# Kernel optimization log

Hardware: AMD Instinct MI355X
Metric: run time of the kernel (lower is better)

Reference implementation:

```python
import jax, jax.numpy as jnp
import numpy as np

D_MODEL = 1024
NUM_HEADS = 16
HEAD_DIM = D_MODEL // NUM_HEADS

def _trunc_normal(key, shape, std=0.02, a=-0.04, b=0.04):
    u = jax.random.truncated_normal(key, a / std, b / std, shape, dtype=jnp.float32)
    return u * std

def setup_inputs() -> dict:
    key = jax.random.key(0)
    kx, kq, kk, kv, ko = jax.random.split(key, 5)
    x = jax.random.normal(kx, (4, 2048, D_MODEL), dtype=jnp.float32)
    Wq = _trunc_normal(kq, (D_MODEL, D_MODEL))
    Wk = _trunc_normal(kk, (D_MODEL, D_MODEL))
    Wv = _trunc_normal(kv, (D_MODEL, D_MODEL))
    Wo = _trunc_normal(ko, (D_MODEL, D_MODEL))
    return {"x": x, "Wq": Wq, "Wk": Wk, "Wv": Wv, "Wo": Wo}

def reference(x, Wq, Wk, Wv, Wo):
    B, S, D = x.shape
    H, Dh = NUM_HEADS, HEAD_DIM
    # projections: x @ W.T
    Q = jnp.einsum('bsd,ed->bse', x, Wq).reshape(B, S, H, Dh).transpose(0, 2, 1, 3)
    K = jnp.einsum('bsd,ed->bse', x, Wk).reshape(B, S, H, Dh).transpose(0, 2, 1, 3)
    V = jnp.einsum('bsd,ed->bse', x, Wv).reshape(B, S, H, Dh).transpose(0, 2, 1, 3)
    scale = 1.0 / jnp.sqrt(jnp.asarray(Dh, dtype=x.dtype))
    scores = jnp.einsum('bhqd,bhkd->bhqk', Q, K) * scale  # [B,H,S,S]
    causal = jnp.tril(jnp.ones((S, S), dtype=bool))  # True where attend allowed
    scores = jnp.where(causal, scores, -jnp.inf)
    attn = jax.nn.softmax(scores, axis=-1)
    ctx = jnp.einsum('bhqk,bhkd->bhqd', attn, V)  # [B,H,S,Dh]
    ctx = ctx.transpose(0, 2, 1, 3).reshape(B, S, D)
    out = jnp.einsum('bsd,ed->bse', ctx, Wo)
    return out
```

## Files before the change

kernel.cpp:

```cpp
#include <hip/hip_runtime.h>

#define D_MODEL 1024
#define SEQ 2048
#define BATCH 4
#define HEADS 16
#define HDIM 64

typedef short bf16x8 __attribute__((ext_vector_type(8)));
typedef float f32x4 __attribute__((ext_vector_type(4)));

#define FENCE() asm volatile("" ::: "memory")

__device__ __forceinline__ unsigned short f2bf(float f) {
  union { float f; unsigned int u; } c; c.f = f;
  unsigned int u = c.u;
  unsigned int r = (u + 0x7FFFu + ((u >> 16) & 1u)) >> 16;
  return (unsigned short)r;
}

__device__ __forceinline__ unsigned int cvt_pk_bf16(float a, float b) {
  unsigned int r;
  asm("v_cvt_pk_bf16_f32 %0, %1, %2" : "=v"(r) : "v"(a), "v"(b));
  return r;
}

__device__ __forceinline__ float exp2_hw(float x) {
  float r;
  asm("v_exp_f32 %0, %1" : "=v"(r) : "v"(x));
  return r;
}

__device__ __forceinline__ void async16(const void* g, const void* lds) {
  __builtin_amdgcn_global_load_lds((const __attribute__((address_space(1))) void*)g,
                                   (__attribute__((address_space(3))) void*)lds, 16, 0, 0);
}

__global__ void cvt_all(const float* __restrict__ x,
                        const float* __restrict__ Wq, const float* __restrict__ Wk,
                        const float* __restrict__ Wv, const float* __restrict__ Wo,
                        unsigned short* __restrict__ xb,
                        unsigned short* __restrict__ Wqkv,
                        unsigned short* __restrict__ Wob) {
  int bid = blockIdx.x;
  const float* s;
  unsigned short* d;
  int i;
  if (bid < 8192) {
    s = x; d = xb; i = bid * 256 + threadIdx.x;
  } else {
    int b = (bid - 8192) >> 10;
    i = ((bid - 8192) & 1023) * 256 + threadIdx.x;
    s = (b == 0) ? Wq : (b == 1) ? Wk : (b == 2) ? Wv : Wo;
    d = (b == 3) ? Wob : (Wqkv + b * (D_MODEL * D_MODEL));
  }
  float4 v = ((const float4*)s)[i];
  ushort4 o;
  o.x = f2bf(v.x); o.y = f2bf(v.y); o.z = f2bf(v.z); o.w = f2bf(v.w);
  ((ushort4*)d)[i] = o;
}

__global__ __launch_bounds__(512, 2) void gemm256qk(
    const unsigned short* __restrict__ A, const unsigned short* __restrict__ Bw,
    unsigned short* __restrict__ Qd, unsigned short* __restrict__ Kd) {
  __shared__ unsigned short At[2][256 * 64];
  __shared__ unsigned short Bt[2][256 * 64];
  const int t = threadIdx.x;
  const int lane = t & 63;
  const int wid = t >> 6;
  const int wm = wid >> 2;
  const int wn = wid & 3;

  const int gx = gridDim.x;
  const int nwg = gridDim.x * gridDim.y;
  int flat = blockIdx.y * gx + blockIdx.x;
  flat = (flat & 7) * (nwg >> 3) + (flat >> 3);
  const int m0 = (flat / gx) * 256;
  const int n0 = (flat % gx) * 256;

  const int K = 1024;
  f32x4 acc[8][4] = {};

  const int srow = t >> 3;
  const int scol = ((t & 7) ^ (srow & 7)) << 3;
  const unsigned short* Ags = A + (size_t)(m0 + srow) * K + scol;
  const unsigned short* Bgs = Bw + (size_t)(n0 + srow) * K + scol;

  const int l15 = lane & 15;
  const int lh = lane >> 4;
  const int rsw = (l15 & 7) << 4;
  const int cb0 = (lh * 16) ^ rsw;
  const int cb1 = (64 + lh * 16) ^ rsw;
  const int aBase = (wm * 128 + l15) * 128;
  const int bBase = (wn * 64 + l15) * 128;

#define STG_A(o, c, kn) async16(Ags + (size_t)(c) * 64 * K + (kn), &At[o][(c) * 4096 + t * 8])
#define STG_B(o, c, kn) async16(Bgs + (size_t)(c) * 64 * K + (kn), &Bt[o][(c) * 4096 + t * 8])

  STG_B(0, 0, 0); STG_B(0, 1, 0); STG_B(0, 2, 0); STG_B(0, 3, 0);
  STG_A(0, 0, 0); STG_A(0, 1, 0); STG_A(0, 2, 0); STG_A(0, 3, 0);
  asm volatile("s_waitcnt vmcnt(0)" ::: "memory");
  __builtin_amdgcn_s_barrier();
  FENCE();

  for (int kt = 0; kt < K; kt += 64) {
    const int s = (kt >> 6) & 1;
    const int o = s ^ 1;
    const int kn = kt + 64;
    const bool more = kn < K;
    const char* Ab = (const char*)&At[s][0];
    const char* Bb = (const char*)&Bt[s][0];

    bf16x8 bfr[4][2];
#pragma unroll
    for (int p = 0; p < 4; ++p) {
      bf16x8 af[2][2];
#pragma unroll
      for (int i = 0; i < 2; ++i) {
        af[i][0] = *(const bf16x8*)(Ab + aBase + (2 * p + i) * 2048 + cb0);
        af[i][1] = *(const bf16x8*)(Ab + aBase + (2 * p + i) * 2048 + cb1);
      }
      if (p == 0) {
#pragma unroll
        for (int fn = 0; fn < 4; ++fn) {
          bfr[fn][0] = *(const bf16x8*)(Bb + bBase + fn * 2048 + cb0);
          bfr[fn][1] = *(const bf16x8*)(Bb + bBase + fn * 2048 + cb1);
        }
        if (more) { STG_B(o, 0, kn); STG_B(o, 1, kn); }
      } else if (p == 1) {
        if (more) { STG_B(o, 2, kn); STG_B(o, 3, kn); }
      } else if (p == 2) {
        if (more) { STG_A(o, 0, kn); STG_A(o, 2, kn); }
      } else {
        if (more) { STG_A(o, 1, kn); STG_A(o, 3, kn); }
      }
      __builtin_amdgcn_s_barrier();
      FENCE();
      __builtin_amdgcn_s_setprio(1);
#pragma unroll
      for (int ks = 0; ks < 2; ++ks)
#pragma unroll
        for (int i = 0; i < 2; ++i)
#pragma unroll
          for (int fn = 0; fn < 4; ++fn)
            acc[2 * p + i][fn] = __builtin_amdgcn_mfma_f32_16x16x32_bf16(
                af[i][ks], bfr[fn][ks], acc[2 * p + i][fn], 0, 0, 0);
      __builtin_amdgcn_s_setprio(0);
      FENCE();
      if (p == 1) {
        if (more) asm volatile("s_waitcnt vmcnt(4)" ::: "memory");
        else      asm volatile("s_waitcnt vmcnt(0)" ::: "memory");
      } else if (p == 3) {
        if (more) asm volatile("s_waitcnt vmcnt(2)" ::: "memory");
        else      asm volatile("s_waitcnt vmcnt(0)" ::: "memory");
      }
      __builtin_amdgcn_s_barrier();
      FENCE();
    }
  }
#undef STG_A
#undef STG_B

#pragma unroll
  for (int fm = 0; fm < 8; ++fm) {
#pragma unroll
    for (int fn = 0; fn < 4; ++fn) {
#pragma unroll
      for (int r = 0; r < 4; ++r) {
        float v = acc[fm][fn][r];
        int m = m0 + wm * 128 + fm * 16 + lh * 4 + r;
        int n = n0 + wn * 64 + fn * 16 + l15;
        int p = n >> 10;
        int h = (n >> 6) & 15;
        int dh = n & 63;
        int b = m >> 11;
        int sx = m & 2047;
        unsigned short* dst = (p == 0) ? Qd : Kd;
        if (p == 0) v *= 0.18033688011112042f;
        dst[(((size_t)(b * HEADS + h)) * SEQ + sx) * HDIM + dh] = f2bf(v);
      }
    }
  }
}

template <int MODE>
__global__ __launch_bounds__(512, 1) void gemm128(
    const unsigned short* __restrict__ A, const unsigned short* __restrict__ Bw,
    int nOfs, unsigned short* __restrict__ Vtd, float* __restrict__ Od) {
  __shared__ unsigned short At[2][128 * 64];
  __shared__ unsigned short Bt[2][256 * 64];
  const int t = threadIdx.x;
  const int lane = t & 63;
  const int wid = t >> 6;
  const int wm = wid >> 1;
  const int wn = wid & 1;

  const int gx = gridDim.x;
  const int nwg = gridDim.x * gridDim.y;
  int flat = blockIdx.y * gx + blockIdx.x;
  flat = (flat & 7) * (nwg >> 3) + (flat >> 3);
  const int m0 = (flat / gx) * 128;
  const int n0 = nOfs + (flat % gx) * 256;

  const int K = 1024;
  f32x4 acc[2][8] = {};

  const int srow = t >> 3;
  const int scol = ((t & 7) ^ (srow & 7)) << 3;
  const unsigned short* Ags = A + (size_t)(m0 + srow) * K + scol;
  const unsigned short* Bgs = Bw + (size_t)(n0 + srow) * K + scol;

  const int l15 = lane & 15;
  const int lh = lane >> 4;
  const int rsw = (l15 & 7) << 4;
  const int cb0 = (lh * 16) ^ rsw;
  const int cb1 = (64 + lh * 16) ^ rsw;
  const int aBase = (wm * 32 + l15) * 128;
  const int bBase = (wn * 128 + l15) * 128;

#define STG_A(o, c, kn) async16(Ags + (size_t)(c) * 64 * K + (kn), &At[o][(c) * 4096 + t * 8])
#define STG_B(o, c, kn) async16(Bgs + (size_t)(c) * 64 * K + (kn), &Bt[o][(c) * 4096 + t * 8])

  STG_A(0, 0, 0); STG_A(0, 1, 0); STG_B(0, 0, 0); STG_B(0, 2, 0);
  STG_B(0, 1, 0); STG_B(0, 3, 0);
  asm volatile("s_waitcnt vmcnt(0)" ::: "memory");
  __builtin_amdgcn_s_barrier();
  FENCE();

  for (int kt = 0; kt < K; kt += 64) {
    const int s = (kt >> 6) & 1;
    const int o = s ^ 1;
    const int kn = kt + 64;
    const bool more = kn < K;
    const char* Ab = (const char*)&At[s][0];
    const char* Bb = (const char*)&Bt[s][0];

    bf16x8 af[2][2];
#pragma unroll
    for (int p = 0; p < 4; ++p) {
      if (p == 0) {
#pragma unroll
        for (int i = 0; i < 2; ++i) {
          af[i][0] = *(const bf16x8*)(Ab + aBase + i * 2048 + cb0);
          af[i][1] = *(const bf16x8*)(Ab + aBase + i * 2048 + cb1);
        }
      }
      bf16x8 bfr[2][2];
#pragma unroll
      for (int j = 0; j < 2; ++j) {
        bfr[j][0] = *(const bf16x8*)(Bb + bBase + (2 * p + j) * 2048 + cb0);
        bfr[j][1] = *(const bf16x8*)(Bb + bBase + (2 * p + j) * 2048 + cb1);
      }
      if (p == 0)      { if (more) { STG_A(o, 0, kn); STG_A(o, 1, kn); } }
      else if (p == 1) { if (more) { STG_B(o, 0, kn); STG_B(o, 2, kn); } }
      else if (p == 2) { if (more) { STG_B(o, 1, kn); STG_B(o, 3, kn); } }
      __builtin_amdgcn_s_barrier();
      FENCE();
      __builtin_amdgcn_s_setprio(1);
#pragma unroll
      for (int ks = 0; ks < 2; ++ks)
#pragma unroll
        for (int i = 0; i < 2; ++i)
#pragma unroll
          for (int j = 0; j < 2; ++j) {
            if (MODE == 1)
              acc[i][2 * p + j] = __builtin_amdgcn_mfma_f32_16x16x32_bf16(
                  bfr[j][ks], af[i][ks], acc[i][2 * p + j], 0, 0, 0);
            else
              acc[i][2 * p + j] = __builtin_amdgcn_mfma_f32_16x16x32_bf16(
                  af[i][ks], bfr[j][ks], acc[i][2 * p + j], 0, 0, 0);
          }
      __builtin_amdgcn_s_setprio(0);
      FENCE();
      if (p == 1) {
        if (more) asm volatile("s_waitcnt vmcnt(4)" ::: "memory");
        else      asm volatile("s_waitcnt vmcnt(0)" ::: "memory");
      } else if (p == 3) {
        if (more) asm volatile("s_waitcnt vmcnt(2)" ::: "memory");
        else      asm volatile("s_waitcnt vmcnt(0)" ::: "memory");
      }
      __builtin_amdgcn_s_barrier();
      FENCE();
    }
  }
#undef STG_A
#undef STG_B

#pragma unroll
  for (int fm = 0; fm < 2; ++fm) {
#pragma unroll
    for (int fn = 0; fn < 8; ++fn) {
#pragma unroll
      for (int r = 0; r < 4; ++r) {
        float v = acc[fm][fn][r];
        if (MODE == 1) {
          int n = n0 + wn * 128 + fn * 16 + lh * 4 + r;
          int m = m0 + wm * 32 + fm * 16 + l15;
          int h = (n >> 6) & 15;
          int d = n & 63;
          int b = m >> 11;
          int s = m & 2047;
          Vtd[(((size_t)(b * HEADS + h)) * HDIM + d) * SEQ + s] = f2bf(v);
        } else {
          int m = m0 + wm * 32 + fm * 16 + lh * 4 + r;
          int n = n0 + wn * 128 + fn * 16 + l15;
          Od[(size_t)m * D_MODEL + n] = v;
        }
      }
    }
  }
}

__global__ __launch_bounds__(256, 3) void attn_fwd(
    const unsigned short* __restrict__ Qg, const unsigned short* __restrict__ Kg,
    const unsigned short* __restrict__ Vtg, unsigned short* __restrict__ Cg) {
  __shared__ unsigned short Kl[128 * 64];
  __shared__ unsigned short Vl[64 * 128];
  __shared__ unsigned short Pl[4][32 * 72];
  char* KlB = (char*)Kl;
  char* VlB = (char*)Vl;

  const int t = threadIdx.x;
  const int lane = t & 63;
  const int wq = t >> 6;
  const int bh = blockIdx.x;
  const int q0 = (15 - blockIdx.y) * 128;
  const size_t base = (size_t)bh * SEQ * HDIM;
  const unsigned short* Qb = Qg + base;
  const unsigned short* Kb = Kg + base;
  const unsigned short* Vb = Vtg + base;
  char* PlB = (char*)&Pl[wq][0];

  const int l15 = lane & 15;
  const int lh = lane >> 4;
  const int qrow = q0 + wq * 32;

  bf16x8 qf[2][2];
#pragma unroll
  for (int fm = 0; fm < 2; ++fm)
#pragma unroll
    for (int ks = 0; ks < 2; ++ks)
      qf[fm][ks] = *(const bf16x8*)&Qb[(size_t)(qrow + fm * 16 + l15) * HDIM +
                                       ks * 32 + lh * 8];

  f32x4 acc[2][4] = {};
  float lpart[2] = {0.f, 0.f};

  const int srow = t >> 3;
  const int sc8 = ((t & 7) ^ (srow & 7)) << 3;
  const int srowV = t >> 4;
  const int scV8 = (((t & 15) ^ (srowV & 7)) << 3);

  const int kv_end = q0 + 128;
  for (int kvb = 0; kvb < kv_end; kvb += 128) {
    __syncthreads();
#pragma unroll
    for (int i = 0; i < 4; ++i)
      async16(Kb + (size_t)(kvb + i * 32 + srow) * HDIM + sc8, &Kl[i * 2048 + t * 8]);
#pragma unroll
    for (int i = 0; i < 4; ++i)
      async16(Vb + (size_t)(i * 16 + srowV) * SEQ + kvb + scV8, &Vl[i * 2048 + t * 8]);
    asm volatile("s_waitcnt vmcnt(0)" ::: "memory");
    __syncthreads();

#pragma unroll
    for (int kh = 0; kh < 2; ++kh) {
      const int kv0 = kvb + kh * 64;
      if (kv0 > qrow + 31) continue;

      f32x4 sfr[2][4] = {};
#pragma unroll
      for (int ks = 0; ks < 2; ++ks) {
        bf16x8 kf[4];
#pragma unroll
        for (int fn = 0; fn < 4; ++fn) {
          int row = kh * 64 + fn * 16 + l15;
          kf[fn] = *(const bf16x8*)&KlB[row * 128 +
                                        ((ks * 64 + lh * 16) ^ ((row & 7) << 4))];
        }
#pragma unroll
        for (int fm = 0; fm < 2; ++fm)
#pragma unroll
          for (int fn = 0; fn < 4; ++fn)
            sfr[fm][fn] = __builtin_amdgcn_mfma_f32_16x16x32_bf16(
                kf[fn], qf[fm][ks], sfr[fm][fn], 0, 0, 0);
      }

      const bool need_mask = (kv0 + 63) > qrow;
#pragma unroll
      for (int fm = 0; fm < 2; ++fm) {
        const int q = qrow + fm * 16 + l15;
        float p[4][4];
#pragma unroll
        for (int fn = 0; fn < 4; ++fn)
#pragma unroll
          for (int r = 0; r < 4; ++r) p[fn][r] = sfr[fm][fn][r];
        if (need_mask) {
#pragma unroll
          for (int fn = 0; fn < 4; ++fn)
#pragma unroll
            for (int r = 0; r < 4; ++r) {
              int key = kv0 + fn * 16 + lh * 4 + r;
              if (key > q) p[fn][r] = -1e30f;
            }
        }
        float st = 0.f;
#pragma unroll
        for (int fn = 0; fn < 4; ++fn)
#pragma unroll
          for (int r = 0; r < 4; ++r) {
            p[fn][r] = exp2_hw(p[fn][r]);
            st += p[fn][r];
          }
        lpart[fm] += st;

#pragma unroll
        for (int fn = 0; fn < 4; ++fn) {
#pragma unroll
          for (int w = 0; w < 2; ++w) {
            unsigned int pk = cvt_pk_bf16(p[fn][2 * w], p[fn][2 * w + 1]);
            *(unsigned int*)&PlB[(fm * 16 + l15) * 144 + fn * 32 + lh * 8 + w * 4] = pk;
          }
        }
      }

#pragma unroll
      for (int ks = 0; ks < 2; ++ks) {
        bf16x8 pf[2], vf[4];
#pragma unroll
        for (int fm = 0; fm < 2; ++fm)
          pf[fm] = *(const bf16x8*)&PlB[(fm * 16 + l15) * 144 + ks * 64 + lh * 16];
#pragma unroll
        for (int fn = 0; fn < 4; ++fn) {
          int row = fn * 16 + l15;
          vf[fn] = *(const bf16x8*)&VlB[row * 256 +
                                        ((kh * 128 + ks * 64 + lh * 16) ^ ((row & 7) << 4))];
        }
#pragma unroll
        for (int fm = 0; fm < 2; ++fm)
#pragma unroll
          for (int fn = 0; fn < 4; ++fn)
            acc[fm][fn] = __builtin_amdgcn_mfma_f32_16x16x32_bf16(
                pf[fm], vf[fn], acc[fm][fn], 0, 0, 0);
      }
    }
  }

  const int b = bh >> 4;
  const int h = bh & 15;
#pragma unroll
  for (int fm = 0; fm < 2; ++fm) {
    float lt = lpart[fm];
    lt += __shfl_xor(lt, 16);
    lt += __shfl_xor(lt, 32);
    float inv = 1.0f / lt;
    float ivr[4];
#pragma unroll
    for (int r = 0; r < 4; ++r) ivr[r] = __shfl(inv, lh * 4 + r);
#pragma unroll
    for (int r = 0; r < 4; ++r) {
      int s = qrow + fm * 16 + lh * 4 + r;
#pragma unroll
      for (int fn = 0; fn < 4; ++fn) {
        int dh = fn * 16 + l15;
        Cg[((size_t)(b * SEQ + s)) * D_MODEL + h * HDIM + dh] =
            f2bf(acc[fm][fn][r] * ivr[r]);
      }
    }
  }
}

extern "C" void kernel_launch(void* const* d_in, const int* in_sizes, int n_in,
                              void* d_out, int out_size, void* d_ws, size_t ws_size,
                              hipStream_t stream) {
  const float* x = (const float*)d_in[0];
  const float* Wq = (const float*)d_in[1];
  const float* Wk = (const float*)d_in[2];
  const float* Wv = (const float*)d_in[3];
  const float* Wo = (const float*)d_in[4];
  float* out = (float*)d_out;

  char* ws = (char*)d_ws;
  unsigned short* xb   = (unsigned short*)(ws);
  unsigned short* Wqkv = (unsigned short*)(ws + (16u << 20));
  unsigned short* Wob  = (unsigned short*)(ws + (22u << 20));
  unsigned short* Qb   = (unsigned short*)(ws + (24u << 20));
  unsigned short* Kb   = (unsigned short*)(ws + (40u << 20));
  unsigned short* Vtb  = (unsigned short*)(ws + (56u << 20));
  unsigned short* Cb   = (unsigned short*)(ws + (72u << 20));

  cvt_all<<<dim3(12288), dim3(256), 0, stream>>>(x, Wq, Wk, Wv, Wo, xb, Wqkv, Wob);

  gemm256qk<<<dim3(8, 32), dim3(512), 0, stream>>>(xb, Wqkv, Qb, Kb);
  gemm128<1><<<dim3(4, 64), dim3(512), 0, stream>>>(xb, Wqkv, 2048, Vtb, nullptr);
  attn_fwd<<<dim3(64, 16), dim3(256), 0, stream>>>(Qb, Kb, Vtb, Cb);
  gemm128<0><<<dim3(4, 64), dim3(512), 0, stream>>>(Cb, Wob, 0, nullptr, out);
}
```

Measured before the change: 151.9 us.

## Load K/V fragments directly from global memory in attention, dropping LDS staging

The attention kernel no longer stages K and V tiles into shared memory with async copies and block barriers. Each wave now reads its K and Vt MFMA fragments straight from global memory, walking only the 64-key chunks its own rows need. Launch bounds rise to four blocks per CU now that LDS use is small. This removes the barriers and the cross-wave sync cost, but each of the four waves fetches the same K/V data separately, leaning on L1/L2 hits and exposing global latency with no prefetch.

```diff
diff --git a/kernel.cpp b/kernel.cpp
--- a/kernel.cpp
+++ b/kernel.cpp
@@ -310,14 +310,10 @@
   }
 }
 
-__global__ __launch_bounds__(256, 3) void attn_fwd(
+__global__ __launch_bounds__(256, 4) void attn_fwd(
     const unsigned short* __restrict__ Qg, const unsigned short* __restrict__ Kg,
     const unsigned short* __restrict__ Vtg, unsigned short* __restrict__ Cg) {
-  __shared__ unsigned short Kl[128 * 64];
-  __shared__ unsigned short Vl[64 * 128];
   __shared__ unsigned short Pl[4][32 * 72];
-  char* KlB = (char*)Kl;
-  char* VlB = (char*)Vl;
 
   const int t = threadIdx.x;
   const int lane = t & 63;
@@ -345,103 +341,80 @@
   f32x4 acc[2][4] = {};
   float lpart[2] = {0.f, 0.f};
 
-  const int srow = t >> 3;
-  const int sc8 = ((t & 7) ^ (srow & 7)) << 3;
-  const int srowV = t >> 4;
-  const int scV8 = (((t & 15) ^ (srowV & 7)) << 3);
-
-  const int kv_end = q0 + 128;
-  for (int kvb = 0; kvb < kv_end; kvb += 128) {
-    __syncthreads();
-#pragma unroll
-    for (int i = 0; i < 4; ++i)
-      async16(Kb + (size_t)(kvb + i * 32 + srow) * HDIM + sc8, &Kl[i * 2048 + t * 8]);
-#pragma unroll
-    for (int i = 0; i < 4; ++i)
-      async16(Vb + (size_t)(i * 16 + srowV) * SEQ + kvb + scV8, &Vl[i * 2048 + t * 8]);
-    asm volatile("s_waitcnt vmcnt(0)" ::: "memory");
-    __syncthreads();
-
-#pragma unroll
-    for (int kh = 0; kh < 2; ++kh) {
-      const int kv0 = kvb + kh * 64;
-      if (kv0 > qrow + 31) continue;
-
-      f32x4 sfr[2][4] = {};
-#pragma unroll
-      for (int ks = 0; ks < 2; ++ks) {
-        bf16x8 kf[4];
-#pragma unroll
-        for (int fn = 0; fn < 4; ++fn) {
-          int row = kh * 64 + fn * 16 + l15;
-          kf[fn] = *(const bf16x8*)&KlB[row * 128 +
-                                        ((ks * 64 + lh * 16) ^ ((row & 7) << 4))];
+  const int nhalf = qrow / 64 + 1;
+  for (int ih = 0; ih < nhalf; ++ih) {
+    const int kv0 = ih * 64;
+
+    f32x4 sfr[2][4] = {};
+#pragma unroll
+    for (int ks = 0; ks < 2; ++ks) {
+      bf16x8 kf[4];
+#pragma unroll
+      for (int fn = 0; fn < 4; ++fn)
+        kf[fn] = *(const bf16x8*)&Kb[(size_t)(kv0 + fn * 16 + l15) * HDIM +
+                                     ks * 32 + lh * 8];
+#pragma unroll
+      for (int fm = 0; fm < 2; ++fm)
+#pragma unroll
+        for (int fn = 0; fn < 4; ++fn)
+          sfr[fm][fn] = __builtin_amdgcn_mfma_f32_16x16x32_bf16(
+              kf[fn], qf[fm][ks], sfr[fm][fn], 0, 0, 0);
+    }
+
+    const bool need_mask = (kv0 + 63) > qrow;
+#pragma unroll
+    for (int fm = 0; fm < 2; ++fm) {
+      const int q = qrow + fm * 16 + l15;
+      float p[4][4];
+#pragma unroll
+      for (int fn = 0; fn < 4; ++fn)
+#pragma unroll
+        for (int r = 0; r < 4; ++r) p[fn][r] = sfr[fm][fn][r];
+      if (need_mask) {
+#pragma unroll
+        for (int fn = 0; fn < 4; ++fn)
+#pragma unroll
+          for (int r = 0; r < 4; ++r) {
+            int key = kv0 + fn * 16 + lh * 4 + r;
+            if (key > q) p[fn][r] = -1e30f;
+          }
+      }
+      float st = 0.f;
+#pragma unroll
+      for (int fn = 0; fn < 4; ++fn)
+#pragma unroll
+        for (int r = 0; r < 4; ++r) {
+          p[fn][r] = exp2_hw(p[fn][r]);
+          st += p[fn][r];
         }
-#pragma unroll
-        for (int fm = 0; fm < 2; ++fm)
-#pragma unroll
-          for (int fn = 0; fn < 4; ++fn)
-            sfr[fm][fn] = __builtin_amdgcn_mfma_f32_16x16x32_bf16(
-                kf[fn], qf[fm][ks], sfr[fm][fn], 0, 0, 0);
-      }
-
-      const bool need_mask = (kv0 + 63) > qrow;
-#pragma unroll
-      for (int fm = 0; fm < 2; ++fm) {
-        const int q = qrow + fm * 16 + l15;
-        float p[4][4];
+      lpart[fm] += st;
+
+#pragma unroll
+      for (int fn = 0; fn < 4; ++fn) {
+#pragma unroll
+        for (int w = 0; w < 2; ++w) {
+          unsigned int pk = cvt_pk_bf16(p[fn][2 * w], p[fn][2 * w + 1]);
+          *(unsigned int*)&PlB[(fm * 16 + l15) * 144 + fn * 32 + lh * 8 + w * 4] = pk;
+        }
+      }
+    }
+
+#pragma unroll
+    for (int ks = 0; ks < 2; ++ks) {
+      bf16x8 pf[2], vf[4];
+#pragma unroll
+      for (int fm = 0; fm < 2; ++fm)
+        pf[fm] = *(const bf16x8*)&PlB[(fm * 16 + l15) * 144 + ks * 64 + lh * 16];
+#pragma unroll
+      for (int fn = 0; fn < 4; ++fn)
+        vf[fn] = *(const bf16x8*)&Vb[(size_t)(fn * 16 + l15) * SEQ + kv0 +
+                                     ks * 32 + lh * 8];
+#pragma unroll
+      for (int fm = 0; fm < 2; ++fm)
 #pragma unroll
         for (int fn = 0; fn < 4; ++fn)
-#pragma unroll
-          for (int r = 0; r < 4; ++r) p[fn][r] = sfr[fm][fn][r];
-        if (need_mask) {
-#pragma unroll
-          for (int fn = 0; fn < 4; ++fn)
-#pragma unroll
-            for (int r = 0; r < 4; ++r) {
-              int key = kv0 + fn * 16 + lh * 4 + r;
-              if (key > q) p[fn][r] = -1e30f;
-            }
-        }
-        float st = 0.f;
-#pragma unroll
-        for (int fn = 0; fn < 4; ++fn)
-#pragma unroll
-          for (int r = 0; r < 4; ++r) {
-            p[fn][r] = exp2_hw(p[fn][r]);
-            st += p[fn][r];
-          }
-        lpart[fm] += st;
-
-#pragma unroll
-        for (int fn = 0; fn < 4; ++fn) {
-#pragma unroll
-          for (int w = 0; w < 2; ++w) {
-            unsigned int pk = cvt_pk_bf16(p[fn][2 * w], p[fn][2 * w + 1]);
-            *(unsigned int*)&PlB[(fm * 16 + l15) * 144 + fn * 32 + lh * 8 + w * 4] = pk;
-          }
-        }
-      }
-
-#pragma unroll
-      for (int ks = 0; ks < 2; ++ks) {
-        bf16x8 pf[2], vf[4];
-#pragma unroll
-        for (int fm = 0; fm < 2; ++fm)
-          pf[fm] = *(const bf16x8*)&PlB[(fm * 16 + l15) * 144 + ks * 64 + lh * 16];
-#pragma unroll
-        for (int fn = 0; fn < 4; ++fn) {
-          int row = fn * 16 + l15;
-          vf[fn] = *(const bf16x8*)&VlB[row * 256 +
-                                        ((kh * 128 + ks * 64 + lh * 16) ^ ((row & 7) << 4))];
-        }
-#pragma unroll
-        for (int fm = 0; fm < 2; ++fm)
-#pragma unroll
-          for (int fn = 0; fn < 4; ++fn)
-            acc[fm][fn] = __builtin_amdgcn_mfma_f32_16x16x32_bf16(
-                pf[fm], vf[fn], acc[fm][fn], 0, 0, 0);
-      }
+          acc[fm][fn] = __builtin_amdgcn_mfma_f32_16x16x32_bf16(
+              pf[fm], vf[fn], acc[fm][fn], 0, 0, 0);
     }
   }
 
```

After: 247.2 us. 1.63x slower.
